# Optimization experiments

Measured on AMD Instinct MI355X. Metric: run time of the kernel, lower is better.

The kernel has to match this reference:

```python
import jax, jax.numpy as jnp
import numpy as np
from jax import lax

INPUT_DIM = 1
HIDDEN_DIM = 256
MAX_SEQ_LEN = 512
BATCH = 8192


def setup_inputs() -> dict:
    key = jax.random.key(0)
    ks = jax.random.split(key, 8)
    s = 1.0 / np.sqrt(HIDDEN_DIM)
    x = jax.random.normal(ks[0], (BATCH, 1, INPUT_DIM), dtype=jnp.float32)
    # torch nn.LSTM params, gate order (i, f, g, o)
    W_ih = jax.random.uniform(ks[1], (4 * HIDDEN_DIM, INPUT_DIM), minval=-s, maxval=s, dtype=jnp.float32)
    W_hh = jax.random.uniform(ks[2], (4 * HIDDEN_DIM, HIDDEN_DIM), minval=-s, maxval=s, dtype=jnp.float32)
    b_ih = jax.random.uniform(ks[3], (4 * HIDDEN_DIM,), minval=-s, maxval=s, dtype=jnp.float32)
    b_hh = jax.random.uniform(ks[4], (4 * HIDDEN_DIM,), minval=-s, maxval=s, dtype=jnp.float32)
    W_fc = jax.random.uniform(ks[5], (1, HIDDEN_DIM), minval=-s, maxval=s, dtype=jnp.float32)
    b_fc = jax.random.uniform(ks[6], (1,), minval=-s, maxval=s, dtype=jnp.float32)
    return {"x": x, "W_ih": W_ih, "W_hh": W_hh, "b_ih": b_ih, "b_hh": b_hh,
            "W_fc": W_fc, "b_fc": b_fc, "max_seq_len": MAX_SEQ_LEN}


def reference(x, W_ih, W_hh, b_ih, b_hh, W_fc, b_fc, max_seq_len):
    B = x.shape[0]
    H = W_hh.shape[1]
    b = b_ih + b_hh  # fold biases once

    def step(carry, _):
        h, c, inp = carry                      # h,c: [B,H]; inp: [B,1]
        gates = inp @ W_ih.T + h @ W_hh.T + b  # [B,4H]
        i, f, g, o = jnp.split(gates, 4, axis=-1)
        c = jax.nn.sigmoid(f) * c + jax.nn.sigmoid(i) * jnp.tanh(g)
        h = jax.nn.sigmoid(o) * jnp.tanh(c)
        d = h @ W_fc.T + b_fc                  # [B,1] depth marker (fc + squeeze of seq dim)
        # torch: outputs[-1].detach() is fed back as next input
        return (h, c, lax.stop_gradient(d)), d

    h0 = jnp.zeros((B, H), dtype=x.dtype)
    c0 = jnp.zeros((B, H), dtype=x.dtype)
    inp0 = x[:, 0, :]                          # [B, input_dim=1]
    _, ds = lax.scan(step, (h0, c0, inp0), None, length=max_seq_len)  # [T,B,1]
    return jnp.moveaxis(ds, 0, 1)              # [B,T,1] == torch.stack(outputs, dim=1)
```

## Files before the change

### kernel.cpp

```cpp
#include <hip/hip_runtime.h>
#include <math.h>

#define HID   256
#define TLEN  512
#define NTHR  1024
#define GSIZE 8
#define NGRP  32
#define BBG   256

#define PLANE_U16 (16 * 8 * 512)
#define HEX_U16   ((size_t)NGRP * 2 * 2 * PLANE_U16)
#define FLAGS_OFF (HEX_U16 * 2)
#define NFLAGS    (NGRP * GSIZE)
#define CNT_OFF   (FLAGS_OFF + (size_t)NFLAGS * 4)
#define WS_NEEDED (CNT_OFF + 8 * 4)

typedef __attribute__((ext_vector_type(8))) short short8;
typedef __attribute__((ext_vector_type(4))) float f32x4;

typedef union {
    float4 f;
    uint4  u;
    short8 s;
} v16u;

static __device__ __forceinline__ unsigned short f2bf_rne(float x) {
    unsigned int u = __float_as_uint(x);
    unsigned int r = (u + 0x7FFFu + ((u >> 16) & 1u)) >> 16;
    return (unsigned short)r;
}
static __device__ __forceinline__ float sigf(float x) {
    return 1.0f / (1.0f + __expf(-x));
}
static __device__ __forceinline__ float tanhf_fast(float x) {
    return 1.0f - 2.0f / (1.0f + __expf(2.0f * x));
}

static __device__ __forceinline__ void issue_l2(const void* p, float4& a) {
    asm volatile("global_load_dwordx4 %0, %1, off sc0"
                 : "=&v"(a) : "v"(p) : "memory");
}
static __device__ __forceinline__ void store_short_l2(void* p, unsigned int v) {
    asm volatile("global_store_short %0, %1, off sc0"
                 :: "v"(p), "v"(v) : "memory");
}
static __device__ __forceinline__ unsigned int load_flag_dev(const unsigned int* p) {
    unsigned int v;
    asm volatile("global_load_dword %0, %1, off sc0 sc1\n\t"
                 "s_waitcnt vmcnt(0)"
                 : "=v"(v) : "v"(p) : "memory");
    return v;
}
static __device__ __forceinline__ void store_flag_dev(unsigned int* p, unsigned int v) {
    asm volatile("global_store_dword %0, %1, off sc0 sc1"
                 :: "v"(p), "v"(v) : "memory");
}

__global__ void init_flags(unsigned int* flags, unsigned int* cnt) {
    int i = blockIdx.x * 256 + threadIdx.x;
    if (i < NFLAGS) store_flag_dev(flags + i, 0u);
    if (i < 8) store_flag_dev(cnt + i, 0u);
}

__global__ __launch_bounds__(NTHR, 4) void lstm_coop11(
    const float* __restrict__ x,
    const float* __restrict__ W_ih,
    const float* __restrict__ W_hh,
    const float* __restrict__ b_ih,
    const float* __restrict__ b_hh,
    const float* __restrict__ W_fc,
    const float* __restrict__ b_fc,
    unsigned short* __restrict__ hexw,
    unsigned int* __restrict__ flags,
    unsigned int* __restrict__ xcnt,
    float* __restrict__ out)
{
    const int tid  = threadIdx.x;
    const int mt   = tid >> 6;
    const int lane = tid & 63;
    const int l15  = lane & 15;
    const int l4   = lane >> 4;

    __shared__ unsigned short whi_s[64 * 512];
    __shared__ unsigned short wlo_s[64 * 512];
    __shared__ unsigned short fhi_s[8 * 512];
    __shared__ unsigned short flo_s[8 * 512];
    __shared__ float wfc_s[HID];
    __shared__ int slot_s;

    if (tid == 0) {
        unsigned int myxcd;
        asm volatile("s_getreg_b32 %0, hwreg(HW_REG_XCC_ID)" : "=s"(myxcd));
        myxcd &= 7u;
        unsigned int s = atomicAdd(&xcnt[myxcd], 1u) & 31u;
        slot_s = (int)(myxcd * 32u + s);
    }
    __syncthreads();
    const int slot = slot_s;
    const int g    = slot >> 3;
    const int p    = slot & 7;
    const int bbase = g * BBG;

    #pragma unroll
    for (int i = 0; i < 4; ++i) {
        int tile = mt * 4 + i;
        int nt = tile >> 3, kc = tile & 7;
        int q = nt >> 1, half = nt & 1;
        int grow = q * 256 + p * 32 + half * 16 + l15;
        int k0 = kc * 32 + l4 * 8;
        const float* src = W_hh + (size_t)grow * HID + k0;
        float4 wa = *(const float4*)src;
        float4 wb = *(const float4*)(src + 4);
        float ff[8] = {wa.x, wa.y, wa.z, wa.w, wb.x, wb.y, wb.z, wb.w};
        short8 hi8, lo8;
        #pragma unroll
        for (int e = 0; e < 8; ++e) {
            unsigned int u = __float_as_uint(ff[e]);
            hi8[e] = (short)(u >> 16);
            float res = ff[e] - __uint_as_float(u & 0xffff0000u);
            lo8[e] = (short)f2bf_rne(res);
        }
        *(short8*)&whi_s[tile * 512 + lane * 8] = hi8;
        *(short8*)&wlo_s[tile * 512 + lane * 8] = lo8;
    }
    if (mt < 8) {
        int kc = mt;
        short8 fh = {0,0,0,0,0,0,0,0};
        short8 fl = {0,0,0,0,0,0,0,0};
        if (l15 == 0) {
            #pragma unroll
            for (int e = 0; e < 8; ++e) {
                float wv = W_fc[kc * 32 + l4 * 8 + e];
                unsigned int u = __float_as_uint(wv);
                fh[e] = (short)(u >> 16);
                float res = wv - __uint_as_float(u & 0xffff0000u);
                fl[e] = (short)f2bf_rne(res);
            }
        }
        *(short8*)&fhi_s[kc * 512 + lane * 8] = fh;
        *(short8*)&flo_s[kc * 512 + lane * 8] = fl;
    }
    if (tid < HID) wfc_s[tid] = W_fc[tid];

    float biasv[8], wihv[8];
    #pragma unroll
    for (int nt = 0; nt < 8; ++nt) {
        int grow = (nt >> 1) * 256 + p * 32 + (nt & 1) * 16 + l15;
        biasv[nt] = b_ih[grow] + b_hh[grow];
        wihv[nt]  = W_ih[grow];
    }
    const float bfc = b_fc[0];

    float c_r[2][4];
    #pragma unroll
    for (int half = 0; half < 2; ++half)
        #pragma unroll
        for (int r = 0; r < 4; ++r) c_r[half][r] = 0.0f;

    unsigned int* flg = flags + g * GSIZE;
    unsigned short* const gbase = hexw + (size_t)g * 4 * PLANE_U16;

    __syncthreads();

    {
        float dreg[4];
        #pragma unroll
        for (int r = 0; r < 4; ++r) dreg[r] = x[bbase + mt * 16 + l4 * 4 + r];

        unsigned short* hiw = gbase + (1 * 2 + 0) * PLANE_U16;
        unsigned short* low = gbase + (1 * 2 + 1) * PLANE_U16;
        #pragma unroll
        for (int half = 0; half < 2; ++half) {
            #pragma unroll
            for (int r = 0; r < 4; ++r) {
                float gi = fmaf(dreg[r], wihv[0 + half], biasv[0 + half]);
                float gf = fmaf(dreg[r], wihv[2 + half], biasv[2 + half]);
                float gg = fmaf(dreg[r], wihv[4 + half], biasv[4 + half]);
                float go = fmaf(dreg[r], wihv[6 + half], biasv[6 + half]);
                float c = fmaf(sigf(gf), c_r[half][r], sigf(gi) * tanhf_fast(gg));
                c_r[half][r] = c;
                float h = sigf(go) * tanhf_fast(c);
                int lane_d = l4 * 4 + r + 16 * (half * 2 + (l15 >> 3));
                int idx = (mt * 8 + p) * 512 + lane_d * 8 + (l15 & 7);
                unsigned int u = __float_as_uint(h);
                store_short_l2(hiw + idx, u >> 16);
                float res = h - __uint_as_float(u & 0xffff0000u);
                store_short_l2(low + idx, (unsigned int)f2bf_rne(res));
            }
        }
        asm volatile("s_waitcnt vmcnt(0)" ::: "memory");
        __syncthreads();
        if (tid == 0) store_flag_dev(&flg[p], 1u);
    }

    #pragma unroll 1
    for (int t = 1; t < TLEN; ++t) {
        if (tid < GSIZE) {
            int guard = 0;
            while (load_flag_dev(&flg[tid]) < (unsigned int)t) {
                if (++guard > (1 << 18)) break;
            }
        }
        __syncthreads();

        const unsigned short* hir = gbase + ((t & 1) * 2 + 0) * PLANE_U16
                                  + (mt * 8) * 512 + lane * 8;
        const unsigned short* lor = gbase + ((t & 1) * 2 + 1) * PLANE_U16
                                  + (mt * 8) * 512 + lane * 8;

        f32x4 acc[8];
        #pragma unroll
        for (int nt = 0; nt < 8; ++nt)
            #pragma unroll
            for (int r = 0; r < 4; ++r) acc[nt][r] = 0.0f;
        f32x4 accd = {0.0f, 0.0f, 0.0f, 0.0f};

        v16u pfh[3], pfl[3];
        issue_l2(hir, pfh[0].f);
        issue_l2(lor, pfl[0].f);
        issue_l2(hir + 512, pfh[1].f);
        issue_l2(lor + 512, pfl[1].f);

        #pragma unroll
        for (int kc = 0; kc < 8; ++kc) {
            if (kc < 6) {
                issue_l2(hir + (kc + 2) * 512, pfh[(kc + 2) % 3].f);
                issue_l2(lor + (kc + 2) * 512, pfl[(kc + 2) % 3].f);
                asm volatile("s_waitcnt vmcnt(4)" ::: "memory");
            } else if (kc == 6) {
                asm volatile("s_waitcnt vmcnt(2)" ::: "memory");
            } else {
                asm volatile("s_waitcnt vmcnt(0)" ::: "memory");
            }
            __builtin_amdgcn_sched_barrier(0);

            const v16u ha = pfh[kc % 3];
            const v16u la = pfl[kc % 3];

            #pragma unroll
            for (int nt = 0; nt < 8; ++nt) {
                short8 bhi = *(const short8*)&whi_s[(nt * 8 + kc) * 512 + lane * 8];
                short8 blo = *(const short8*)&wlo_s[(nt * 8 + kc) * 512 + lane * 8];
                acc[nt] = __builtin_amdgcn_mfma_f32_16x16x32_bf16(ha.s, bhi, acc[nt], 0, 0, 0);
                acc[nt] = __builtin_amdgcn_mfma_f32_16x16x32_bf16(la.s, bhi, acc[nt], 0, 0, 0);
                acc[nt] = __builtin_amdgcn_mfma_f32_16x16x32_bf16(ha.s, blo, acc[nt], 0, 0, 0);
            }
            {
                short8 fh = *(const short8*)&fhi_s[kc * 512 + lane * 8];
                short8 fl = *(const short8*)&flo_s[kc * 512 + lane * 8];
                accd = __builtin_amdgcn_mfma_f32_16x16x32_bf16(ha.s, fh, accd, 0, 0, 0);
                accd = __builtin_amdgcn_mfma_f32_16x16x32_bf16(la.s, fh, accd, 0, 0, 0);
                accd = __builtin_amdgcn_mfma_f32_16x16x32_bf16(ha.s, fl, accd, 0, 0, 0);
            }
        }

        if (p == 0 && l15 == 0) {
            #pragma unroll
            for (int r = 0; r < 4; ++r)
                out[(size_t)(bbase + mt * 16 + l4 * 4 + r) * TLEN + (t - 1)] = accd[r] + bfc;
        }
        float dreg[4];
        #pragma unroll
        for (int r = 0; r < 4; ++r)
            dreg[r] = __shfl(accd[r], lane & 48) + bfc;

        unsigned short* hiw = gbase + ((((t + 1) & 1)) * 2 + 0) * PLANE_U16;
        unsigned short* low = gbase + ((((t + 1) & 1)) * 2 + 1) * PLANE_U16;
        #pragma unroll
        for (int half = 0; half < 2; ++half) {
            #pragma unroll
            for (int r = 0; r < 4; ++r) {
                float gi = acc[0 + half][r] + fmaf(dreg[r], wihv[0 + half], biasv[0 + half]);
                float gf = acc[2 + half][r] + fmaf(dreg[r], wihv[2 + half], biasv[2 + half]);
                float gg = acc[4 + half][r] + fmaf(dreg[r], wihv[4 + half], biasv[4 + half]);
                float go = acc[6 + half][r] + fmaf(dreg[r], wihv[6 + half], biasv[6 + half]);
                float c = fmaf(sigf(gf), c_r[half][r], sigf(gi) * tanhf_fast(gg));
                c_r[half][r] = c;
                float h = sigf(go) * tanhf_fast(c);
                int lane_d = l4 * 4 + r + 16 * (half * 2 + (l15 >> 3));
                int idx = (mt * 8 + p) * 512 + lane_d * 8 + (l15 & 7);
                unsigned int u = __float_as_uint(h);
                store_short_l2(hiw + idx, u >> 16);
                float res = h - __uint_as_float(u & 0xffff0000u);
                store_short_l2(low + idx, (unsigned int)f2bf_rne(res));
            }
        }
        asm volatile("s_waitcnt vmcnt(0)" ::: "memory");
        __syncthreads();
        if (tid == 0) store_flag_dev(&flg[p], (unsigned int)(t + 1));
    }

    {
        if (tid < GSIZE) {
            int guard = 0;
            while (load_flag_dev(&flg[tid]) < (unsigned int)TLEN) {
                if (++guard > (1 << 18)) break;
            }
        }
        __syncthreads();
        if (p == 0) {
            const unsigned short* hir = gbase + (0 * 2 + 0) * PLANE_U16
                                      + (mt * 8) * 512 + lane * 8;
            const unsigned short* lor = gbase + (0 * 2 + 1) * PLANE_U16
                                      + (mt * 8) * 512 + lane * 8;
            float dsum = 0.0f;
            #pragma unroll
            for (int kc = 0; kc < 8; ++kc) {
                v16u va, vb;
                issue_l2(hir + kc * 512, va.f);
                issue_l2(lor + kc * 512, vb.f);
                asm volatile("s_waitcnt vmcnt(0)" ::: "memory");
                __builtin_amdgcn_sched_barrier(0);
                const float* wf = &wfc_s[kc * 32 + l4 * 8];
                unsigned int uu[4] = {va.u.x, va.u.y, va.u.z, va.u.w};
                unsigned int ll[4] = {vb.u.x, vb.u.y, vb.u.z, vb.u.w};
                #pragma unroll
                for (int i = 0; i < 4; ++i) {
                    float h0 = __uint_as_float(uu[i] << 16)
                             + __uint_as_float(ll[i] << 16);
                    float h1 = __uint_as_float(uu[i] & 0xffff0000u)
                             + __uint_as_float(ll[i] & 0xffff0000u);
                    dsum = fmaf(h0, wf[2 * i + 0], dsum);
                    dsum = fmaf(h1, wf[2 * i + 1], dsum);
                }
            }
            dsum += __shfl_xor(dsum, 16);
            dsum += __shfl_xor(dsum, 32);
            if (lane < 16)
                out[(size_t)(bbase + mt * 16 + lane) * TLEN + (TLEN - 1)] = dsum + bfc;
        }
    }
}

#define BB 32
__global__ __launch_bounds__(NTHR, 4) void lstm_mfma7(
    const float* __restrict__ x, const float* __restrict__ W_ih,
    const float* __restrict__ W_hh, const float* __restrict__ b_ih,
    const float* __restrict__ b_hh, const float* __restrict__ W_fc,
    const float* __restrict__ b_fc, float* __restrict__ out)
{
    const int tid = threadIdx.x;
    const int wave = tid >> 6;
    const int lane = tid & 63;
    const int l15 = lane & 15;
    const int l4 = lane >> 4;
    const int bbase = blockIdx.x * BB;

    __shared__ unsigned short hhi[2][16 * 512];
    __shared__ unsigned short hlo[2][16 * 512];
    __shared__ float dpart[16][BB];
    __shared__ float inp_s[BB];

    for (int i = tid; i < 16 * 512; i += NTHR) { hhi[0][i] = 0; hlo[0][i] = 0; }
    if (tid < BB) inp_s[tid] = x[bbase + tid];

    float biasv[4], wihv[4];
    #pragma unroll
    for (int q = 0; q < 4; ++q) {
        int gg = 256 * q + 16 * wave + l15;
        biasv[q] = b_ih[gg] + b_hh[gg];
        wihv[q] = W_ih[gg];
    }
    const float wfc = W_fc[16 * wave + l15];
    const float bfc = b_fc[0];
    const float* __restrict__ wrow = W_hh + (size_t)(16 * wave + l15) * HID + l4 * 8;
    const int kc_w = wave >> 1;
    const int kwhi = (wave & 1) * 2 + (l15 >> 3);
    const int elemw = l15 & 7;

    float c_r[2][4];
    #pragma unroll
    for (int m = 0; m < 2; ++m)
        #pragma unroll
        for (int r = 0; r < 4; ++r) c_r[m][r] = 0.0f;
    __syncthreads();

    #pragma unroll 1
    for (int t = 0; t < TLEN; ++t) {
        const int p = t & 1;
        f32x4 acc[2][4];
        {
            float dv[2][4];
            #pragma unroll
            for (int m = 0; m < 2; ++m)
                #pragma unroll
                for (int r = 0; r < 4; ++r) dv[m][r] = inp_s[16 * m + 4 * l4 + r];
            #pragma unroll
            for (int m = 0; m < 2; ++m)
                #pragma unroll
                for (int q = 0; q < 4; ++q)
                    #pragma unroll
                    for (int r = 0; r < 4; ++r)
                        acc[m][q][r] = fmaf(dv[m][r], wihv[q], biasv[q]);
        }
        #pragma unroll
        for (int kc = 0; kc < 8; ++kc) {
            short8 ahi[2], alo[2];
            #pragma unroll
            for (int m = 0; m < 2; ++m) {
                int aoff = (m * 8 + kc) * 512 + lane * 8;
                ahi[m] = *(const short8*)&hhi[p][aoff];
                alo[m] = *(const short8*)&hlo[p][aoff];
            }
            #pragma unroll
            for (int q = 0; q < 4; ++q) {
                const float* src = wrow + (size_t)q * 256 * HID + kc * 32;
                float4 wa = *(const float4*)src;
                float4 wb = *(const float4*)(src + 4);
                float ff[8] = {wa.x, wa.y, wa.z, wa.w, wb.x, wb.y, wb.z, wb.w};
                short8 bhi, blo;
                #pragma unroll
                for (int e = 0; e < 8; ++e) {
                    unsigned int u = __float_as_uint(ff[e]);
                    bhi[e] = (short)(u >> 16);
                    float res = ff[e] - __uint_as_float(u & 0xffff0000u);
                    blo[e] = (short)(__float_as_uint(res) >> 16);
                }
                #pragma unroll
                for (int m = 0; m < 2; ++m) {
                    acc[m][q] = __builtin_amdgcn_mfma_f32_16x16x32_bf16(ahi[m], bhi, acc[m][q], 0, 0, 0);
                    acc[m][q] = __builtin_amdgcn_mfma_f32_16x16x32_bf16(alo[m], bhi, acc[m][q], 0, 0, 0);
                    acc[m][q] = __builtin_amdgcn_mfma_f32_16x16x32_bf16(ahi[m], blo, acc[m][q], 0, 0, 0);
                }
            }
        }
        #pragma unroll
        for (int m = 0; m < 2; ++m) {
            #pragma unroll
            for (int r = 0; r < 4; ++r) {
                float gi = acc[m][0][r];
                float gf = acc[m][1][r];
                float gg = acc[m][2][r];
                float go = acc[m][3][r];
                float c = fmaf(sigf(gf), c_r[m][r], sigf(gi) * tanhf_fast(gg));
                c_r[m][r] = c;
                float h = sigf(go) * tanhf_fast(c);
                unsigned short hh = f2bf_rne(h);
                float hres = h - __uint_as_float(__float_as_uint(h) & 0xffff0000u);
                int haddr = (m * 8 + kc_w) * 512 + ((4 * l4 + r) + 16 * kwhi) * 8 + elemw;
                hhi[p ^ 1][haddr] = hh;
                hlo[p ^ 1][haddr] = f2bf_rne(hres);
                float s = h * wfc;
                s += __shfl_xor(s, 1);
                s += __shfl_xor(s, 2);
                s += __shfl_xor(s, 4);
                s += __shfl_xor(s, 8);
                if (l15 == 0) dpart[wave][16 * m + 4 * l4 + r] = s;
            }
        }
        __syncthreads();
        if (tid < BB) {
            float s = bfc;
            #pragma unroll
            for (int w = 0; w < 16; ++w) s += dpart[w][tid];
            inp_s[tid] = s;
            out[(size_t)(bbase + tid) * TLEN + t] = s;
        }
        __syncthreads();
    }
}

extern "C" void kernel_launch(void* const* d_in, const int* in_sizes, int n_in,
                              void* d_out, int out_size, void* d_ws, size_t ws_size,
                              hipStream_t stream) {
    const float* x    = (const float*)d_in[0];
    const float* W_ih = (const float*)d_in[1];
    const float* W_hh = (const float*)d_in[2];
    const float* b_ih = (const float*)d_in[3];
    const float* b_hh = (const float*)d_in[4];
    const float* W_fc = (const float*)d_in[5];
    const float* b_fc = (const float*)d_in[6];
    float* out = (float*)d_out;

    const int BATCH = in_sizes[0];

    if (ws_size >= WS_NEEDED) {
        unsigned int* flags = (unsigned int*)((char*)d_ws + FLAGS_OFF);
        unsigned int* xcnt  = (unsigned int*)((char*)d_ws + CNT_OFF);
        init_flags<<<1, 256, 0, stream>>>(flags, xcnt);
        lstm_coop11<<<BATCH / BBG * GSIZE, NTHR, 0, stream>>>(
            x, W_ih, W_hh, b_ih, b_hh, W_fc, b_fc,
            (unsigned short*)d_ws, flags, xcnt, out);
    } else {
        lstm_mfma7<<<BATCH / BB, NTHR, 0, stream>>>(
            x, W_ih, W_hh, b_ih, b_hh, W_fc, b_fc, out);
    }
}
```

Measured before the change: 7.068 ms.

## Retile per-wave MFMA work to 2 M-tiles by 4 gate N-tiles

Each wave now covers two 16-row batch tiles and one half of the gate columns, where before it covered one batch tile and all eight N-tiles. Every weight fragment read from LDS therefore feeds two MFMAs, halving the LDS weight traffic per wave, while the h fragments are loaded twice across the pair of waves sharing an M-tile. This adds per-wave global loads of h and doubles the FC-dot MFMAs (now computed redundantly by both wn waves), and it raises the register count for prefetch buffers.

```diff
diff --git a/kernel.cpp b/kernel.cpp
--- a/kernel.cpp
+++ b/kernel.cpp
@@ -62,7 +62,7 @@
     if (i < 8) store_flag_dev(cnt + i, 0u);
 }
 
-__global__ __launch_bounds__(NTHR, 4) void lstm_coop11(
+__global__ __launch_bounds__(NTHR, 4) void lstm_coop14(
     const float* __restrict__ x,
     const float* __restrict__ W_ih,
     const float* __restrict__ W_hh,
@@ -76,7 +76,9 @@
     float* __restrict__ out)
 {
     const int tid  = threadIdx.x;
-    const int mt   = tid >> 6;
+    const int wv   = tid >> 6;
+    const int wm   = wv >> 1;
+    const int wn   = wv & 1;
     const int lane = tid & 63;
     const int l15  = lane & 15;
     const int l4   = lane >> 4;
@@ -103,7 +105,7 @@
 
     #pragma unroll
     for (int i = 0; i < 4; ++i) {
-        int tile = mt * 4 + i;
+        int tile = wv * 4 + i;
         int nt = tile >> 3, kc = tile & 7;
         int q = nt >> 1, half = nt & 1;
         int grow = q * 256 + p * 32 + half * 16 + l15;
@@ -123,17 +125,17 @@
         *(short8*)&whi_s[tile * 512 + lane * 8] = hi8;
         *(short8*)&wlo_s[tile * 512 + lane * 8] = lo8;
     }
-    if (mt < 8) {
-        int kc = mt;
+    if (wv < 8) {
+        int kc = wv;
         short8 fh = {0,0,0,0,0,0,0,0};
         short8 fl = {0,0,0,0,0,0,0,0};
         if (l15 == 0) {
             #pragma unroll
             for (int e = 0; e < 8; ++e) {
-                float wv = W_fc[kc * 32 + l4 * 8 + e];
-                unsigned int u = __float_as_uint(wv);
+                float wvv = W_fc[kc * 32 + l4 * 8 + e];
+                unsigned int u = __float_as_uint(wvv);
                 fh[e] = (short)(u >> 16);
-                float res = wv - __uint_as_float(u & 0xffff0000u);
+                float res = wvv - __uint_as_float(u & 0xffff0000u);
                 fl[e] = (short)f2bf_rne(res);
             }
         }
@@ -142,46 +144,44 @@
     }
     if (tid < HID) wfc_s[tid] = W_fc[tid];
 
-    float biasv[8], wihv[8];
+    float biasv[4], wihv[4];
     #pragma unroll
-    for (int nt = 0; nt < 8; ++nt) {
-        int grow = (nt >> 1) * 256 + p * 32 + (nt & 1) * 16 + l15;
-        biasv[nt] = b_ih[grow] + b_hh[grow];
-        wihv[nt]  = W_ih[grow];
+    for (int q = 0; q < 4; ++q) {
+        int grow = q * 256 + p * 32 + wn * 16 + l15;
+        biasv[q] = b_ih[grow] + b_hh[grow];
+        wihv[q]  = W_ih[grow];
     }
     const float bfc = b_fc[0];
 
     float c_r[2][4];
     #pragma unroll
-    for (int half = 0; half < 2; ++half)
-        #pragma unroll
-        for (int r = 0; r < 4; ++r) c_r[half][r] = 0.0f;
+    for (int mtl = 0; mtl < 2; ++mtl)
+        #pragma unroll
+        for (int r = 0; r < 4; ++r) c_r[mtl][r] = 0.0f;
 
     unsigned int* flg = flags + g * GSIZE;
     unsigned short* const gbase = hexw + (size_t)g * 4 * PLANE_U16;
 
+    const int stbase = 16 * (wn * 2 + (l15 >> 3)) * 8 + (l15 & 7);
+
     __syncthreads();
 
     {
-        float dreg[4];
-        #pragma unroll
-        for (int r = 0; r < 4; ++r) dreg[r] = x[bbase + mt * 16 + l4 * 4 + r];
-
         unsigned short* hiw = gbase + (1 * 2 + 0) * PLANE_U16;
         unsigned short* low = gbase + (1 * 2 + 1) * PLANE_U16;
         #pragma unroll
-        for (int half = 0; half < 2; ++half) {
+        for (int mtl = 0; mtl < 2; ++mtl) {
             #pragma unroll
             for (int r = 0; r < 4; ++r) {
-                float gi = fmaf(dreg[r], wihv[0 + half], biasv[0 + half]);
-                float gf = fmaf(dreg[r], wihv[2 + half], biasv[2 + half]);
-                float gg = fmaf(dreg[r], wihv[4 + half], biasv[4 + half]);
-                float go = fmaf(dreg[r], wihv[6 + half], biasv[6 + half]);
-                float c = fmaf(sigf(gf), c_r[half][r], sigf(gi) * tanhf_fast(gg));
-                c_r[half][r] = c;
+                float dv = x[bbase + (wm * 2 + mtl) * 16 + l4 * 4 + r];
+                float gi = fmaf(dv, wihv[0], biasv[0]);
+                float gf = fmaf(dv, wihv[1], biasv[1]);
+                float gg = fmaf(dv, wihv[2], biasv[2]);
+                float go = fmaf(dv, wihv[3], biasv[3]);
+                float c = fmaf(sigf(gf), c_r[mtl][r], sigf(gi) * tanhf_fast(gg));
+                c_r[mtl][r] = c;
                 float h = sigf(go) * tanhf_fast(c);
-                int lane_d = l4 * 4 + r + 16 * (half * 2 + (l15 >> 3));
-                int idx = (mt * 8 + p) * 512 + lane_d * 8 + (l15 & 7);
+                int idx = ((wm * 2 + mtl) * 8 + p) * 512 + (l4 * 4 + r) * 8 + stbase;
                 unsigned int u = __float_as_uint(h);
                 store_short_l2(hiw + idx, u >> 16);
                 float res = h - __uint_as_float(u & 0xffff0000u);
@@ -203,82 +203,109 @@
         }
         __syncthreads();
 
-        const unsigned short* hir = gbase + ((t & 1) * 2 + 0) * PLANE_U16
-                                  + (mt * 8) * 512 + lane * 8;
-        const unsigned short* lor = gbase + ((t & 1) * 2 + 1) * PLANE_U16
-                                  + (mt * 8) * 512 + lane * 8;
-
-        f32x4 acc[8];
-        #pragma unroll
-        for (int nt = 0; nt < 8; ++nt)
-            #pragma unroll
-            for (int r = 0; r < 4; ++r) acc[nt][r] = 0.0f;
-        f32x4 accd = {0.0f, 0.0f, 0.0f, 0.0f};
-
-        v16u pfh[3], pfl[3];
-        issue_l2(hir, pfh[0].f);
-        issue_l2(lor, pfl[0].f);
-        issue_l2(hir + 512, pfh[1].f);
-        issue_l2(lor + 512, pfl[1].f);
+        const unsigned short* hir = gbase + ((t & 1) * 2 + 0) * PLANE_U16 + lane * 8;
+        const unsigned short* lor = gbase + ((t & 1) * 2 + 1) * PLANE_U16 + lane * 8;
+
+        f32x4 acc[2][4];
+        #pragma unroll
+        for (int mtl = 0; mtl < 2; ++mtl)
+            #pragma unroll
+            for (int q = 0; q < 4; ++q)
+                #pragma unroll
+                for (int r = 0; r < 4; ++r) acc[mtl][q][r] = 0.0f;
+        f32x4 accd[2];
+        #pragma unroll
+        for (int mtl = 0; mtl < 2; ++mtl)
+            #pragma unroll
+            for (int r = 0; r < 4; ++r) accd[mtl][r] = 0.0f;
+
+        v16u pfh[3][2], pfl[3][2];
+        #pragma unroll
+        for (int k0 = 0; k0 < 2; ++k0) {
+            #pragma unroll
+            for (int mtl = 0; mtl < 2; ++mtl) {
+                int off = ((wm * 2 + mtl) * 8 + k0) * 512;
+                issue_l2(hir + off, pfh[k0][mtl].f);
+                issue_l2(lor + off, pfl[k0][mtl].f);
+            }
+        }
 
         #pragma unroll
         for (int kc = 0; kc < 8; ++kc) {
             if (kc < 6) {
-                issue_l2(hir + (kc + 2) * 512, pfh[(kc + 2) % 3].f);
-                issue_l2(lor + (kc + 2) * 512, pfl[(kc + 2) % 3].f);
+                #pragma unroll
+                for (int mtl = 0; mtl < 2; ++mtl) {
+                    int off = ((wm * 2 + mtl) * 8 + (kc + 2)) * 512;
+                    issue_l2(hir + off, pfh[(kc + 2) % 3][mtl].f);
+                    issue_l2(lor + off, pfl[(kc + 2) % 3][mtl].f);
+                }
+                asm volatile("s_waitcnt vmcnt(8)" ::: "memory");
+            } else if (kc == 6) {
                 asm volatile("s_waitcnt vmcnt(4)" ::: "memory");
-            } else if (kc == 6) {
-                asm volatile("s_waitcnt vmcnt(2)" ::: "memory");
             } else {
                 asm volatile("s_waitcnt vmcnt(0)" ::: "memory");
             }
             __builtin_amdgcn_sched_barrier(0);
 
-            const v16u ha = pfh[kc % 3];
-            const v16u la = pfl[kc % 3];
-
-            #pragma unroll
-            for (int nt = 0; nt < 8; ++nt) {
-                short8 bhi = *(const short8*)&whi_s[(nt * 8 + kc) * 512 + lane * 8];
-                short8 blo = *(const short8*)&wlo_s[(nt * 8 + kc) * 512 + lane * 8];
-                acc[nt] = __builtin_amdgcn_mfma_f32_16x16x32_bf16(ha.s, bhi, acc[nt], 0, 0, 0);
-                acc[nt] = __builtin_amdgcn_mfma_f32_16x16x32_bf16(la.s, bhi, acc[nt], 0, 0, 0);
-                acc[nt] = __builtin_amdgcn_mfma_f32_16x16x32_bf16(ha.s, blo, acc[nt], 0, 0, 0);
+            const v16u ha0 = pfh[kc % 3][0];
+            const v16u la0 = pfl[kc % 3][0];
+            const v16u ha1 = pfh[kc % 3][1];
+            const v16u la1 = pfl[kc % 3][1];
+
+            #pragma unroll
+            for (int q = 0; q < 4; ++q) {
+                int tile = (q * 2 + wn) * 8 + kc;
+                short8 bhi = *(const short8*)&whi_s[tile * 512 + lane * 8];
+                short8 blo = *(const short8*)&wlo_s[tile * 512 + lane * 8];
+                acc[0][q] = __builtin_amdgcn_mfma_f32_16x16x32_bf16(ha0.s, bhi, acc[0][q], 0, 0, 0);
+                acc[0][q] = __builtin_amdgcn_mfma_f32_16x16x32_bf16(la0.s, bhi, acc[0][q], 0, 0, 0);
+                acc[0][q] = __builtin_amdgcn_mfma_f32_16x16x32_bf16(ha0.s, blo, acc[0][q], 0, 0, 0);
+                acc[1][q] = __builtin_amdgcn_mfma_f32_16x16x32_bf16(ha1.s, bhi, acc[1][q], 0, 0, 0);
+                acc[1][q] = __builtin_amdgcn_mfma_f32_16x16x32_bf16(la1.s, bhi, acc[1][q], 0, 0, 0);
+                acc[1][q] = __builtin_amdgcn_mfma_f32_16x16x32_bf16(ha1.s, blo, acc[1][q], 0, 0, 0);
             }
             {
                 short8 fh = *(const short8*)&fhi_s[kc * 512 + lane * 8];
                 short8 fl = *(const short8*)&flo_s[kc * 512 + lane * 8];
-                accd = __builtin_amdgcn_mfma_f32_16x16x32_bf16(ha.s, fh, accd, 0, 0, 0);
-                accd = __builtin_amdgcn_mfma_f32_16x16x32_bf16(la.s, fh, accd, 0, 0, 0);
-                accd = __builtin_amdgcn_mfma_f32_16x16x32_bf16(ha.s, fl, accd, 0, 0, 0);
-            }
-        }
-
-        if (p == 0 && l15 == 0) {
+                accd[0] = __builtin_amdgcn_mfma_f32_16x16x32_bf16(ha0.s, fh, accd[0], 0, 0, 0);
+                accd[0] = __builtin_amdgcn_mfma_f32_16x16x32_bf16(la0.s, fh, accd[0], 0, 0, 0);
+                accd[0] = __builtin_amdgcn_mfma_f32_16x16x32_bf16(ha0.s, fl, accd[0], 0, 0, 0);
+                accd[1] = __builtin_amdgcn_mfma_f32_16x16x32_bf16(ha1.s, fh, accd[1], 0, 0, 0);
+                accd[1] = __builtin_amdgcn_mfma_f32_16x16x32_bf16(la1.s, fh, accd[1], 0, 0, 0);
+                accd[1] = __builtin_amdgcn_mfma_f32_16x16x32_bf16(ha1.s, fl, accd[1], 0, 0, 0);
+            }
+        }
+
+        if (p == 0 && wn == 0 && l15 == 0) {
+            #pragma unroll
+            for (int mtl = 0; mtl < 2; ++mtl)
+                #pragma unroll
+                for (int r = 0; r < 4; ++r)
+                    out[(size_t)(bbase + (wm * 2 + mtl) * 16 + l4 * 4 + r) * TLEN + (t - 1)]
+                        = accd[mtl][r] + bfc;
+        }
+        float dreg[2][4];
+        #pragma unroll
+        for (int mtl = 0; mtl < 2; ++mtl)
             #pragma unroll
             for (int r = 0; r < 4; ++r)
-                out[(size_t)(bbase + mt * 16 + l4 * 4 + r) * TLEN + (t - 1)] = accd[r] + bfc;
-        }
-        float dreg[4];
-        #pragma unroll
-        for (int r = 0; r < 4; ++r)
-            dreg[r] = __shfl(accd[r], lane & 48) + bfc;
+                dreg[mtl][r] = __shfl(accd[mtl][r], lane & 48) + bfc;
 
         unsigned short* hiw = gbase + ((((t + 1) & 1)) * 2 + 0) * PLANE_U16;
         unsigned short* low = gbase + ((((t + 1) & 1)) * 2 + 1) * PLANE_U16;
         #pragma unroll
-        for (int half = 0; half < 2; ++half) {
+        for (int mtl = 0; mtl < 2; ++mtl) {
             #pragma unroll
             for (int r = 0; r < 4; ++r) {
-                float gi = acc[0 + half][r] + fmaf(dreg[r], wihv[0 + half], biasv[0 + half]);
-                float gf = acc[2 + half][r] + fmaf(dreg[r], wihv[2 + half], biasv[2 + half]);
-                float gg = acc[4 + half][r] + fmaf(dreg[r], wihv[4 + half], biasv[4 + half]);
-                float go = acc[6 + half][r] + fmaf(dreg[r], wihv[6 + half], biasv[6 + half]);
-                float c = fmaf(sigf(gf), c_r[half][r], sigf(gi) * tanhf_fast(gg));
-                c_r[half][r] = c;
+                float dv = dreg[mtl][r];
+                float gi = acc[mtl][0][r] + fmaf(dv, wihv[0], biasv[0]);
+                float gf = acc[mtl][1][r] + fmaf(dv, wihv[1], biasv[1]);
+                float gg = acc[mtl][2][r] + fmaf(dv, wihv[2], biasv[2]);
+                float go = acc[mtl][3][r] + fmaf(dv, wihv[3], biasv[3]);
+                float c = fmaf(sigf(gf), c_r[mtl][r], sigf(gi) * tanhf_fast(gg));
+                c_r[mtl][r] = c;
                 float h = sigf(go) * tanhf_fast(c);
-                int lane_d = l4 * 4 + r + 16 * (half * 2 + (l15 >> 3));
-                int idx = (mt * 8 + p) * 512 + lane_d * 8 + (l15 & 7);
+                int idx = ((wm * 2 + mtl) * 8 + p) * 512 + (l4 * 4 + r) * 8 + stbase;
                 unsigned int u = __float_as_uint(h);
                 store_short_l2(hiw + idx, u >> 16);
                 float res = h - __uint_as_float(u & 0xffff0000u);
@@ -299,6 +326,7 @@
         }
         __syncthreads();
         if (p == 0) {
+            const int mt = wv;
             const unsigned short* hir = gbase + (0 * 2 + 0) * PLANE_U16
                                       + (mt * 8) * 512 + lane * 8;
             const unsigned short* lor = gbase + (0 * 2 + 1) * PLANE_U16
@@ -478,7 +506,7 @@
         unsigned int* flags = (unsigned int*)((char*)d_ws + FLAGS_OFF);
         unsigned int* xcnt  = (unsigned int*)((char*)d_ws + CNT_OFF);
         init_flags<<<1, 256, 0, stream>>>(flags, xcnt);
-        lstm_coop11<<<BATCH / BBG * GSIZE, NTHR, 0, stream>>>(
+        lstm_coop14<<<BATCH / BBG * GSIZE, NTHR, 0, stream>>>(
             x, W_ih, W_hh, b_ih, b_hh, W_fc, b_fc,
             (unsigned short*)d_ws, flags, xcnt, out);
     } else {
```

Result: slower. 10.24 ms (+44.9%).
